# Kernel tuning notes

Hardware: AMD Instinct MI355X
Metric: run time of the kernel (lower is better)

## Reference

```python
import jax, jax.numpy as jnp
import numpy as np

B, T, E, V, H = 2, 2048, 1024, 2048, 8
KD, HD = E // H, V // H  # key_dim=128, head_dim=256
EPS = 1e-6


def rotate_every_two(x):
    x1 = x[..., ::2]
    x2 = x[..., 1::2]
    return jnp.stack((-x2, x1), axis=-1).reshape(x.shape)


def theta_shift(x, sin, cos):
    return x * cos + rotate_every_two(x) * sin


def setup_inputs() -> dict:
    key = jax.random.key(0)
    ks = jax.random.split(key, 8)
    x = jax.random.normal(ks[0], (B, T, E), dtype=jnp.float32)
    angle = jnp.arange(T, dtype=jnp.float32)[:, None] * (1.0 / (10000.0 ** (jnp.repeat(jnp.arange(KD // 2, dtype=jnp.float32), 2) * 2.0 / KD)))
    sin = jnp.sin(angle)  # [T, KD]
    cos = jnp.cos(angle)
    # RetNet per-head causal decay mask: decay_h = 1 - 2^(-5-h)
    decay = 1.0 - 2.0 ** (-5.0 - jnp.arange(H, dtype=jnp.float32))  # [H]
    idx = jnp.arange(T, dtype=jnp.float32)
    diff = idx[:, None] - idx[None, :]  # n - m
    causal = diff >= 0
    mask = jnp.where(causal[None], jnp.exp(jnp.where(causal, diff, 0.0)[None] * jnp.log(decay)[:, None, None]), 0.0)  # [H,T,T]
    g = 2 ** (-2.5)
    Wq = jax.random.normal(ks[1], (E, E), dtype=jnp.float32) * (g * np.sqrt(2.0 / (E + E)))
    Wk = jax.random.normal(ks[2], (E, E), dtype=jnp.float32) * (g * np.sqrt(2.0 / (E + E)))
    Wv = jax.random.normal(ks[3], (E, V), dtype=jnp.float32) * (g * np.sqrt(2.0 / (E + V)))
    Wg = jax.random.normal(ks[4], (E, V), dtype=jnp.float32) * (g * np.sqrt(2.0 / (E + V)))
    Wo = jax.random.normal(ks[5], (V, E), dtype=jnp.float32) * np.sqrt(2.0 / (V + E))
    return {"x": x, "sin": sin, "cos": cos, "mask": mask,
            "Wq": Wq, "Wk": Wk, "Wv": Wv, "Wg": Wg, "Wo": Wo}


def reference(x, sin, cos, mask, Wq, Wk, Wv, Wg, Wo):
    b, t, _ = x.shape
    scaling = KD ** -0.5
    q = (x @ Wq).reshape(b, t, H, KD).transpose(0, 2, 1, 3)  # [B,H,T,KD]
    k = (x @ Wk * scaling).reshape(b, t, H, KD).transpose(0, 2, 1, 3)
    v = x @ Wv  # [B,T,V]
    g = x @ Wg
    qr = theta_shift(q, sin, cos)
    kr = theta_shift(k, sin, cos)
    vr = v.reshape(b, t, H, HD).transpose(0, 2, 1, 3)  # [B,H,T,HD]
    qk = jnp.einsum('bhsk,bhtk->bhst', qr, kr) * mask  # [B,H,T,T]
    denom = jnp.clip(jnp.abs(jax.lax.stop_gradient(qk).sum(-1, keepdims=True)), 1.0, None)
    qk = qk / denom
    out = jnp.einsum('bhst,bhtd->bhsd', qk, vr)  # [B,H,T,HD]
    out = out.transpose(0, 2, 1, 3)  # [B,T,H,HD]
    # RMSNorm over head_dim, no affine
    out = out * jax.lax.rsqrt(jnp.mean(out * out, axis=-1, keepdims=True) + EPS)
    out = out.reshape(b, t, H * HD)
    out = jax.nn.silu(g) * out
    return out @ Wo  # [B,T,E]
```

## Files before the change

### kernel.cpp

```cpp
#include <hip/hip_runtime.h>
#include <hip/hip_bf16.h>


#define B_ 2
#define T_ 2048
#define E_ 1024
#define V_ 2048
#define H_ 8
#define KD_ 128
#define HD_ 256
#define M_ 4096

typedef __attribute__((ext_vector_type(8))) short bf16x8;
typedef __attribute__((ext_vector_type(4))) float f32x4;

__device__ __forceinline__ float u2f(unsigned short u) {
    return __uint_as_float(((unsigned)u) << 16);
}
__device__ __forceinline__ unsigned short f2bu(float f) {
    unsigned x = __float_as_uint(f);
    return (unsigned short)((x + 0x7fffu + ((x >> 16) & 1u)) >> 16);
}

typedef const __attribute__((address_space(1))) void gas_t;
typedef __attribute__((address_space(3))) void las_t;
__device__ __forceinline__ void gl_lds16(const void* g, void* l) {
    __builtin_amdgcn_global_load_lds((gas_t*)g, (las_t*)l, 16, 0, 0);
}

__global__ __launch_bounds__(256) void conv_x_kernel(
    const float* __restrict__ x, unsigned short* __restrict__ xb)
{
    const size_t i = ((size_t)blockIdx.x * 256 + threadIdx.x) * 8;
    float4 a = *(const float4*)(x + i);
    float4 c = *(const float4*)(x + i + 4);
    *(ushort4*)(xb + i)     = make_ushort4(f2bu(a.x), f2bu(a.y), f2bu(a.z), f2bu(a.w));
    *(ushort4*)(xb + i + 4) = make_ushort4(f2bu(c.x), f2bu(c.y), f2bu(c.z), f2bu(c.w));
}

__global__ __launch_bounds__(256) void transW4_kernel(
    const float* __restrict__ Wq, const float* __restrict__ Wk,
    const float* __restrict__ Wv, const float* __restrict__ Wg,
    unsigned short* __restrict__ Wt)
{
    const int z = blockIdx.z;
    const float* W; int N; int rofs;
    if (z == 0)      { W = Wq; N = 1024; rofs = 0; }
    else if (z == 1) { W = Wk; N = 1024; rofs = 1024; }
    else if (z == 2) { W = Wv; N = 2048; rofs = 2048; }
    else             { W = Wg; N = 2048; rofs = 4096; }
    const int n0 = blockIdx.x * 64;
    if (n0 >= N) return;
    const int k0 = blockIdx.y * 64;

    __shared__ float tl[64][65];
    const int tid = threadIdx.x;
    #pragma unroll
    for (int i = 0; i < 4; ++i) {
        int kr = i * 16 + (tid >> 4);
        int nc = (tid & 15) * 4;
        float4 v = *(const float4*)(W + (size_t)(k0 + kr) * N + n0 + nc);
        tl[kr][nc] = v.x; tl[kr][nc + 1] = v.y; tl[kr][nc + 2] = v.z; tl[kr][nc + 3] = v.w;
    }
    __syncthreads();
    #pragma unroll
    for (int i = 0; i < 4; ++i) {
        int nr = i * 16 + (tid >> 4);
        int kc = (tid & 15) * 4;
        ushort4 u = make_ushort4(f2bu(tl[kc + 0][nr]), f2bu(tl[kc + 1][nr]),
                                 f2bu(tl[kc + 2][nr]), f2bu(tl[kc + 3][nr]));
        *(ushort4*)(Wt + (size_t)(rofs + n0 + nr) * E_ + k0 + kc) = u;
    }
}

__global__ __launch_bounds__(256) void transW_kernel(
    const float* __restrict__ W, unsigned short* __restrict__ Wt, int K, int N)
{
    __shared__ float tl[64][65];
    const int tid = threadIdx.x;
    const int n0 = blockIdx.x * 64, k0 = blockIdx.y * 64;
    #pragma unroll
    for (int i = 0; i < 4; ++i) {
        int kr = i * 16 + (tid >> 4);
        int nc = (tid & 15) * 4;
        float4 v = *(const float4*)(W + (size_t)(k0 + kr) * N + n0 + nc);
        tl[kr][nc] = v.x; tl[kr][nc + 1] = v.y; tl[kr][nc + 2] = v.z; tl[kr][nc + 3] = v.w;
    }
    __syncthreads();
    #pragma unroll
    for (int i = 0; i < 4; ++i) {
        int nr = i * 16 + (tid >> 4);
        int kc = (tid & 15) * 4;
        ushort4 u = make_ushort4(f2bu(tl[kc + 0][nr]), f2bu(tl[kc + 1][nr]),
                                 f2bu(tl[kc + 2][nr]), f2bu(tl[kc + 3][nr]));
        *(ushort4*)(Wt + (size_t)(n0 + nr) * K + k0 + kc) = u;
    }
}

__global__ __launch_bounds__(256) void transV_kernel(
    const unsigned short* __restrict__ vb, unsigned short* __restrict__ vt)
{
    __shared__ unsigned short tl[64][68];
    const int tid = threadIdx.x;
    const int t0 = blockIdx.x * 64, c0 = blockIdx.y * 64, b = blockIdx.z;
    #pragma unroll
    for (int i = 0; i < 4; ++i) {
        int tr = i * 16 + (tid >> 4);
        int cc = (tid & 15) * 4;
        ushort4 v = *(const ushort4*)(vb + (size_t)(b * T_ + t0 + tr) * V_ + c0 + cc);
        tl[tr][cc] = v.x; tl[tr][cc + 1] = v.y; tl[tr][cc + 2] = v.z; tl[tr][cc + 3] = v.w;
    }
    __syncthreads();
    #pragma unroll
    for (int i = 0; i < 4; ++i) {
        int cr = i * 16 + (tid >> 4);
        int tc = (tid & 15) * 4;
        ushort4 u = make_ushort4(tl[tc + 0][cr], tl[tc + 1][cr], tl[tc + 2][cr], tl[tc + 3][cr]);
        *(ushort4*)(vt + (size_t)(b * V_ + c0 + cr) * T_ + t0 + tc) = u;
    }
}

#define GSTAGE(BUF, K0)                                                        \
    {                                                                          \
        _Pragma("unroll")                                                      \
        for (int i = 0; i < 4; ++i) {                                          \
            int r = i * 32 + srow;                                             \
            int cb = scolb ^ ((r & 7) << 4);                                   \
            gl_lds16((const char*)(A  + (size_t)(rowBase + r) * K + (K0)) + cb,\
                     Asm[BUF] + i * 4096 + w * 1024);                          \
            gl_lds16((const char*)(Bt + (size_t)(colBase + r) * K + (K0)) + cb,\
                     Bsm[BUF] + i * 4096 + w * 1024);                          \
        }                                                                      \
    }

#define GCOMPUTE(BUF)                                                          \
    {                                                                          \
        _Pragma("unroll")                                                      \
        for (int kk = 0; kk < 2; ++kk) {                                       \
            const int cb = kk * 64 + (l >> 4) * 16;                            \
            bf16x8 a[4], b[4];                                                 \
            _Pragma("unroll")                                                  \
            for (int m = 0; m < 4; ++m) {                                      \
                int r = wr * 64 + m * 16 + (l & 15);                           \
                a[m] = *(const bf16x8*)(Asm[BUF] + r * 128 + (cb ^ ((r & 7) << 4))); \
            }                                                                  \
            _Pragma("unroll")                                                  \
            for (int n = 0; n < 4; ++n) {                                      \
                int r = wc * 64 + n * 16 + (l & 15);                           \
                b[n] = *(const bf16x8*)(Bsm[BUF] + r * 128 + (cb ^ ((r & 7) << 4))); \
            }                                                                  \
            _Pragma("unroll")                                                  \
            for (int m = 0; m < 4; ++m)                                        \
                _Pragma("unroll")                                              \
                for (int n = 0; n < 4; ++n)                                    \
                    acc[m][n] = __builtin_amdgcn_mfma_f32_16x16x32_bf16(a[m], b[n], acc[m][n], 0, 0, 0); \
        }                                                                      \
    }

#define GEMM_PIPELINE_LOOP                                                     \
    GSTAGE(0, 0)                                                               \
    const int nk = K / 64;                                                     \
    for (int kt = 0; kt < nk; ++kt) {                                          \
        const int cur = kt & 1;                                                \
        if (kt + 1 < nk) {                                                     \
            GSTAGE(1 - cur, (kt + 1) * 64)                                     \
            asm volatile("s_waitcnt vmcnt(8)" ::: "memory");                   \
        } else {                                                               \
            asm volatile("s_waitcnt vmcnt(0)" ::: "memory");                   \
        }                                                                      \
        __builtin_amdgcn_s_barrier();                                          \
        __builtin_amdgcn_sched_barrier(0);                                     \
        GCOMPUTE(cur)                                                          \
        __builtin_amdgcn_s_barrier();                                          \
        __builtin_amdgcn_sched_barrier(0);                                     \
    }

__global__ __launch_bounds__(256) void gemm_qkvg_kernel(
    const unsigned short* __restrict__ A,
    const unsigned short* __restrict__ Bt,
    unsigned short* __restrict__ qb,
    unsigned short* __restrict__ kb,
    unsigned short* __restrict__ vb,
    unsigned short* __restrict__ gb)
{
    const int K = E_;
    __shared__ __align__(16) char Asm[2][128 * 64 * 2];
    __shared__ __align__(16) char Bsm[2][128 * 64 * 2];
    const int tid = threadIdx.x;
    const int l = tid & 63;
    const int w = tid >> 6;
    const int wr = w >> 1, wc = w & 1;
    const int rowBase = blockIdx.y * 128;
    const int colBase = blockIdx.x * 128;
    const int srow = tid >> 3;
    const int scolb = (tid & 7) * 16;

    f32x4 acc[4][4] = {};

    GEMM_PIPELINE_LOOP

    const int colW = colBase + wc * 64;
    unsigned short* dst;
    int cofs, stride;
    if (colW < 1024)      { dst = qb; cofs = 0;    stride = E_; }
    else if (colW < 2048) { dst = kb; cofs = 1024; stride = E_; }
    else if (colW < 4096) { dst = vb; cofs = 2048; stride = V_; }
    else                  { dst = gb; cofs = 4096; stride = V_; }
    #pragma unroll
    for (int m = 0; m < 4; ++m)
        #pragma unroll
        for (int n = 0; n < 4; ++n)
            #pragma unroll
            for (int r = 0; r < 4; ++r) {
                int row = rowBase + wr * 64 + m * 16 + (l >> 4) * 4 + r;
                int col = colW + n * 16 + (l & 15);
                float f = acc[m][n][r];
                if (!isfinite(f)) f = 0.f;
                dst[(size_t)row * stride + (col - cofs)] = f2bu(f);
            }
}

__global__ __launch_bounds__(256) void gemm_wo_kernel(
    const unsigned short* __restrict__ A,
    const unsigned short* __restrict__ Bt,
    float* __restrict__ C)
{
    const int K = V_;
    __shared__ __align__(16) char Asm[2][64 * 128];
    __shared__ __align__(16) char Bsm[2][128 * 128];
    const int tid = threadIdx.x;
    const int l = tid & 63;
    const int w = tid >> 6;
    const int wr = w >> 1, wc = w & 1;
    const int rowBase = blockIdx.y * 64;
    const int colBase = blockIdx.x * 128;
    const int srow = tid >> 3;
    const int scolb = (tid & 7) * 16;

    f32x4 acc[2][4] = {};

#define WSTAGE(BUF, K0)                                                        \
    {                                                                          \
        _Pragma("unroll")                                                      \
        for (int i = 0; i < 2; ++i) {                                          \
            int r = i * 32 + srow;                                             \
            int cb = scolb ^ ((r & 7) << 4);                                   \
            gl_lds16((const char*)(A + (size_t)(rowBase + r) * K + (K0)) + cb, \
                     Asm[BUF] + i * 4096 + w * 1024);                          \
        }                                                                      \
        _Pragma("unroll")                                                      \
        for (int i = 0; i < 4; ++i) {                                          \
            int r = i * 32 + srow;                                             \
            int cb = scolb ^ ((r & 7) << 4);                                   \
            gl_lds16((const char*)(Bt + (size_t)(colBase + r) * K + (K0)) + cb,\
                     Bsm[BUF] + i * 4096 + w * 1024);                          \
        }                                                                      \
    }

    WSTAGE(0, 0)
    const int nk = K / 64;
    for (int kt = 0; kt < nk; ++kt) {
        const int cur = kt & 1;
        if (kt + 1 < nk) {
            WSTAGE(1 - cur, (kt + 1) * 64)
            asm volatile("s_waitcnt vmcnt(6)" ::: "memory");
        } else {
            asm volatile("s_waitcnt vmcnt(0)" ::: "memory");
        }
        __builtin_amdgcn_s_barrier();
        __builtin_amdgcn_sched_barrier(0);
        #pragma unroll
        for (int kk = 0; kk < 2; ++kk) {
            const int cb = kk * 64 + (l >> 4) * 16;
            bf16x8 a[2], b[4];
            #pragma unroll
            for (int m = 0; m < 2; ++m) {
                int r = wr * 32 + m * 16 + (l & 15);
                a[m] = *(const bf16x8*)(Asm[cur] + r * 128 + (cb ^ ((r & 7) << 4)));
            }
            #pragma unroll
            for (int n = 0; n < 4; ++n) {
                int r = wc * 64 + n * 16 + (l & 15);
                b[n] = *(const bf16x8*)(Bsm[cur] + r * 128 + (cb ^ ((r & 7) << 4)));
            }
            #pragma unroll
            for (int m = 0; m < 2; ++m)
                #pragma unroll
                for (int n = 0; n < 4; ++n)
                    acc[m][n] = __builtin_amdgcn_mfma_f32_16x16x32_bf16(a[m], b[n], acc[m][n], 0, 0, 0);
        }
        __builtin_amdgcn_s_barrier();
        __builtin_amdgcn_sched_barrier(0);
    }
#undef WSTAGE

    #pragma unroll
    for (int m = 0; m < 2; ++m)
        #pragma unroll
        for (int n = 0; n < 4; ++n)
            #pragma unroll
            for (int r = 0; r < 4; ++r) {
                int row = rowBase + wr * 32 + m * 16 + (l >> 4) * 4 + r;
                int col = colBase + wc * 64 + n * 16 + (l & 15);
                float f = acc[m][n][r];
                if (!isfinite(f)) f = 0.f;
                C[(size_t)row * E_ + col] = f;
            }
}

__global__ __launch_bounds__(256) void theta2_kernel(
    unsigned short* __restrict__ qb,
    unsigned short* __restrict__ kb,
    const float* __restrict__ sinp, const float* __restrict__ cosp)
{
    unsigned short* qk = blockIdx.y ? kb : qb;
    const float scale = blockIdx.y ? 0.088388347648318447f : 1.0f;
    const int i = blockIdx.x * 256 + threadIdx.x;
    const int pe = i & (E_ / 2 - 1);
    const int bt = i >> 9;
    const int t = bt & (T_ - 1);
    const int e0 = pe << 1;
    const int d0 = e0 & (KD_ - 1);
    const size_t base = (size_t)bt * E_ + e0;
    const float q0 = u2f(qk[base]);
    const float q1 = u2f(qk[base + 1]);
    const int sb = t * KD_ + d0;
    const float s0 = sinp[sb], s1 = sinp[sb + 1];
    const float c0 = cosp[sb], c1 = cosp[sb + 1];
    qk[base]     = f2bu((q0 * c0 - q1 * s0) * scale);
    qk[base + 1] = f2bu((q1 * c1 + q0 * s1) * scale);
}

#define STAGE_K(BUF, T0)                                                       \
    {                                                                          \
        _Pragma("unroll")                                                      \
        for (int i = 0; i < 4; ++i) {                                          \
            int r = i * 16 + (tid >> 4);                                       \
            int cb = ((tid & 15) * 16) ^ ((r & 7) << 4);                       \
            gl_lds16((const char*)(kb + (size_t)(b * T_ + (T0) + r) * E_ + h * KD_) + cb, \
                     Ks[BUF] + i * 4096 + w * 1024);                           \
        }                                                                      \
    }

#define STAGE_V(T0)                                                            \
    {                                                                          \
        _Pragma("unroll")                                                      \
        for (int i = 0; i < 8; ++i) {                                          \
            int r = i * 32 + (tid >> 3);                                       \
            int cb = ((tid & 7) * 16) ^ ((r & 7) << 4);                        \
            gl_lds16((const char*)(vt + (size_t)((b * H_ + h) * HD_ + r) * T_ + (T0)) + cb, \
                     Vs + i * 4096 + w * 1024);                                \
        }                                                                      \
    }

__global__ __launch_bounds__(256) void retention_mfma_kernel(
    const unsigned short* __restrict__ qb,
    const unsigned short* __restrict__ kb,
    const unsigned short* __restrict__ vt,
    const unsigned short* __restrict__ g,
    unsigned short* __restrict__ ao)
{
    __shared__ __align__(16) char Ks[2][64 * 128 * 2];
    __shared__ __align__(16) char Vs[256 * 64 * 2];
    __shared__ __align__(16) char Ps[64 * 64 * 2];
    __shared__ float rsum_lds[64];
    __shared__ float rsq_lds[4][64];
    const int tid = threadIdx.x;
    const int l = tid & 63;
    const int w = tid >> 6;
    const int orig = (int)blockIdx.x;
    const int xcd  = orig & 7;
    const int pos  = orig >> 3;
    const int slot = pos >> 5;
    const int cu   = pos & 31;
    const int half = cu >> 4;
    const int c15  = cu & 15;
    const int bh   = xcd * 2 + half;
    const int chunk = slot ? c15 : (31 - c15);
    const int b = bh >> 3, h = bh & 7;
    const int s0 = chunk * 64;
    const float ld = logf(1.f - exp2f(-5.f - (float)h));

    float es[4], etl[4];
    #pragma unroll
    for (int r = 0; r < 4; ++r)
        es[r] = __expf((float)(s0 + w * 16 + (l >> 4) * 4 + r) * ld);
    #pragma unroll
    for (int n = 0; n < 4; ++n)
        etl[n] = __expf(-(float)(n * 16 + (l & 15)) * ld);
    const float Dm64 = __expf(-64.f * ld);
    float etb = 1.f;

    bf16x8 qf[4];
    {
        const char* qp = (const char*)(qb + (size_t)(b * T_ + s0 + w * 16 + (l & 15)) * E_ + h * KD_);
        #pragma unroll
        for (int kk = 0; kk < 4; ++kk)
            qf[kk] = *(const bf16x8*)(qp + kk * 64 + (l >> 4) * 16);
    }

    f32x4 oacc[4][4] = {};
    float rs[4] = {0.f, 0.f, 0.f, 0.f};

    const int nt = chunk + 1;
    STAGE_K(0, 0)

    for (int t = 0; t < nt; ++t) {
        const int cur = t & 1;
        const int t0 = t * 64;
        STAGE_V(t0)
        if (t + 1 < nt) {
            STAGE_K(1 - cur, t0 + 64)
            asm volatile("s_waitcnt vmcnt(12)" ::: "memory");
        } else {
            asm volatile("s_waitcnt vmcnt(8)" ::: "memory");
        }
        __builtin_amdgcn_s_barrier();
        __builtin_amdgcn_sched_barrier(0);

        f32x4 sacc[4] = {};
        #pragma unroll
        for (int kk = 0; kk < 4; ++kk) {
            const int cb = kk * 64 + (l >> 4) * 16;
            #pragma unroll
            for (int n = 0; n < 4; ++n) {
                int r = n * 16 + (l & 15);
                bf16x8 kf = *(const bf16x8*)(Ks[cur] + r * 256 + (cb ^ ((r & 7) << 4)));
                sacc[n] = __builtin_amdgcn_mfma_f32_16x16x32_bf16(qf[kk], kf, sacc[n], 0, 0, 0);
            }
        }
        float et[4];
        #pragma unroll
        for (int n = 0; n < 4; ++n) et[n] = etb * etl[n];
        etb *= Dm64;
        float rsp[4] = {0.f, 0.f, 0.f, 0.f};
        #pragma unroll
        for (int n = 0; n < 4; ++n)
            #pragma unroll
            for (int r = 0; r < 4; ++r) {
                int qrow = w * 16 + (l >> 4) * 4 + r;
                int tcol = n * 16 + (l & 15);
                int d = (s0 + qrow) - (t0 + tcol);
                float pm = (d >= 0) ? sacc[n][r] * (es[r] * et[n]) : 0.f;
                rsp[r] += pm;
                *(unsigned short*)(Ps + qrow * 128 + ((tcol * 2) ^ ((qrow & 7) << 4))) = f2bu(pm);
            }
        #pragma unroll
        for (int r = 0; r < 4; ++r) {
            float vv = rsp[r];
            vv += __shfl_xor(vv, 1, 16);
            vv += __shfl_xor(vv, 2, 16);
            vv += __shfl_xor(vv, 4, 16);
            vv += __shfl_xor(vv, 8, 16);
            rs[r] += vv;
        }
        if (t + 1 < nt) {
            asm volatile("s_waitcnt vmcnt(4) lgkmcnt(0)" ::: "memory");
        } else {
            asm volatile("s_waitcnt vmcnt(0) lgkmcnt(0)" ::: "memory");
        }
        __builtin_amdgcn_s_barrier();
        __builtin_amdgcn_sched_barrier(0);
        #pragma unroll
        for (int kk = 0; kk < 2; ++kk) {
            const int cb = kk * 64 + (l >> 4) * 16;
            bf16x8 pf[4];
            #pragma unroll
            for (int m = 0; m < 4; ++m) {
                int pr = m * 16 + (l & 15);
                pf[m] = *(const bf16x8*)(Ps + pr * 128 + (cb ^ ((pr & 7) << 4)));
            }
            #pragma unroll
            for (int n = 0; n < 4; ++n) {
                int r = w * 64 + n * 16 + (l & 15);
                bf16x8 vf = *(const bf16x8*)(Vs + r * 128 + (cb ^ ((r & 7) << 4)));
                #pragma unroll
                for (int m = 0; m < 4; ++m)
                    oacc[m][n] = __builtin_amdgcn_mfma_f32_16x16x32_bf16(pf[m], vf, oacc[m][n], 0, 0, 0);
            }
        }
        __builtin_amdgcn_s_barrier();
        __builtin_amdgcn_sched_barrier(0);
    }

    #pragma unroll
    for (int r = 0; r < 4; ++r)
        if ((l & 15) == 0) rsum_lds[w * 16 + (l >> 4) * 4 + r] = rs[r];
    __syncthreads();

    #pragma unroll
    for (int m = 0; m < 4; ++m)
        #pragma unroll
        for (int r = 0; r < 4; ++r) {
            const int row = m * 16 + (l >> 4) * 4 + r;
            const float inv = 1.f / fmaxf(fabsf(rsum_lds[row]), 1.f);
            float ps = 0.f;
            #pragma unroll
            for (int n = 0; n < 4; ++n) {
                float o = oacc[m][n][r] * inv;
                ps += o * o;
            }
            ps += __shfl_xor(ps, 1, 16);
            ps += __shfl_xor(ps, 2, 16);
            ps += __shfl_xor(ps, 4, 16);
            ps += __shfl_xor(ps, 8, 16);
            if ((l & 15) == 0) rsq_lds[w][row] = ps;
        }
    __syncthreads();

    #pragma unroll
    for (int m = 0; m < 4; ++m)
        #pragma unroll
        for (int r = 0; r < 4; ++r) {
            const int row = m * 16 + (l >> 4) * 4 + r;
            const float inv = 1.f / fmaxf(fabsf(rsum_lds[row]), 1.f);
            const float tot = rsq_lds[0][row] + rsq_lds[1][row] + rsq_lds[2][row] + rsq_lds[3][row];
            const float scale = rsqrtf(tot * (1.0f / HD_) + 1e-6f) * inv;
            #pragma unroll
            for (int n = 0; n < 4; ++n) {
                const int col = h * HD_ + w * 64 + n * 16 + (l & 15);
                const float gv = u2f(g[(size_t)(b * T_ + s0 + row) * V_ + col]);
                const float silu = gv / (1.f + __expf(-gv));
                float f = oacc[m][n][r] * scale * silu;
                if (!isfinite(f)) f = 0.f;
                ao[(size_t)(b * T_ + s0 + row) * V_ + col] = f2bu(f);
            }
        }
}

extern "C" void kernel_launch(void* const* d_in, const int* in_sizes, int n_in,
                              void* d_out, int out_size, void* d_ws, size_t ws_size,
                              hipStream_t stream)
{
    const float* x    = (const float*)d_in[0];
    const float* sinp = (const float*)d_in[1];
    const float* cosp = (const float*)d_in[2];
    const float* Wq   = (const float*)d_in[4];
    const float* Wk   = (const float*)d_in[5];
    const float* Wv   = (const float*)d_in[6];
    const float* Wg   = (const float*)d_in[7];
    const float* Wo   = (const float*)d_in[8];
    float* out = (float*)d_out;

    unsigned short* xb = (unsigned short*)d_out;
    unsigned short* qb = xb + (size_t)M_ * E_;

    char* ws = (char*)d_ws;
    unsigned short* kb  = (unsigned short*)(ws + 0);
    unsigned short* vb  = (unsigned short*)(ws + 8388608);
    unsigned short* gb  = (unsigned short*)(ws + 25165824);
    unsigned short* wt  = (unsigned short*)(ws + 41943040);
    unsigned short* vt  = (unsigned short*)(ws + 54525952);
    unsigned short* aob = (unsigned short*)(ws + 71303168);
    unsigned short* wot = (unsigned short*)(ws + 88080384);

    dim3 blk(256);
    conv_x_kernel<<<M_ * E_ / 8 / 256, blk, 0, stream>>>(x, xb);

    transW4_kernel<<<dim3(32, 16, 4), blk, 0, stream>>>(Wq, Wk, Wv, Wg, wt);

    gemm_qkvg_kernel<<<dim3(48, 32), blk, 0, stream>>>(xb, wt, qb, kb, vb, gb);

    theta2_kernel<<<dim3(M_ * E_ / 2 / 256, 2), blk, 0, stream>>>(qb, kb, sinp, cosp);

    transV_kernel<<<dim3(32, 32, B_), blk, 0, stream>>>(vb, vt);

    retention_mfma_kernel<<<dim3(512), blk, 0, stream>>>(qb, kb, vt, gb, aob);

    transW_kernel<<<dim3(16, 32), blk, 0, stream>>>(Wo, wot, V_, E_);
    gemm_wo_kernel<<<dim3(8, 64), blk, 0, stream>>>(aob, wot, out);
}
```

Before: 203.3 us.

## Transpose retention MFMA layout so query index lives in lanes, vectorize P and output stores

```diff
diff --git a/kernel.cpp b/kernel.cpp
--- a/kernel.cpp
+++ b/kernel.cpp
@@ -353,7 +353,7 @@
         }                                                                      \
     }
 
-__global__ __launch_bounds__(256) void retention_mfma_kernel(
+__global__ __launch_bounds__(256, 2) void retention_mfma_kernel(
     const unsigned short* __restrict__ qb,
     const unsigned short* __restrict__ kb,
     const unsigned short* __restrict__ vt,
@@ -362,12 +362,14 @@
 {
     __shared__ __align__(16) char Ks[2][64 * 128 * 2];
     __shared__ __align__(16) char Vs[256 * 64 * 2];
-    __shared__ __align__(16) char Ps[64 * 64 * 2];
-    __shared__ float rsum_lds[64];
-    __shared__ float rsq_lds[4][64];
+    __shared__ __align__(16) char Pq[64 * 64 * 2];
+    __shared__ float rsum_p[4][64];
+    __shared__ float rsq_p[4][64];
     const int tid = threadIdx.x;
     const int l = tid & 63;
     const int w = tid >> 6;
+    const int g_ = l >> 4;
+    const int q15 = l & 15;
     const int orig = (int)blockIdx.x;
     const int xcd  = orig & 7;
     const int pos  = orig >> 3;
@@ -381,25 +383,27 @@
     const int s0 = chunk * 64;
     const float ld = logf(1.f - exp2f(-5.f - (float)h));
 
-    float es[4], etl[4];
+    float es[4];
+    #pragma unroll
+    for (int qb2 = 0; qb2 < 4; ++qb2)
+        es[qb2] = __expf((float)(s0 + qb2 * 16 + q15) * ld);
+    float etl[4];
     #pragma unroll
     for (int r = 0; r < 4; ++r)
-        es[r] = __expf((float)(s0 + w * 16 + (l >> 4) * 4 + r) * ld);
-    #pragma unroll
-    for (int n = 0; n < 4; ++n)
-        etl[n] = __expf(-(float)(n * 16 + (l & 15)) * ld);
+        etl[r] = __expf(-(float)(w * 16 + 4 * g_ + r) * ld);
     const float Dm64 = __expf(-64.f * ld);
     float etb = 1.f;
 
-    bf16x8 qf[4];
-    {
-        const char* qp = (const char*)(qb + (size_t)(b * T_ + s0 + w * 16 + (l & 15)) * E_ + h * KD_);
+    bf16x8 qf[4][4];
+    #pragma unroll
+    for (int qb2 = 0; qb2 < 4; ++qb2) {
+        const char* qp = (const char*)(qb + (size_t)(b * T_ + s0 + qb2 * 16 + q15) * E_ + h * KD_);
         #pragma unroll
         for (int kk = 0; kk < 4; ++kk)
-            qf[kk] = *(const bf16x8*)(qp + kk * 64 + (l >> 4) * 16);
-    }
-
-    f32x4 oacc[4][4] = {};
+            qf[qb2][kk] = *(const bf16x8*)(qp + kk * 64 + g_ * 16);
+    }
+
+    f32x4 oaccT[4][4] = {};
     float rs[4] = {0.f, 0.f, 0.f, 0.f};
 
     const int nt = chunk + 1;
@@ -419,40 +423,39 @@
         __builtin_amdgcn_sched_barrier(0);
 
         f32x4 sacc[4] = {};
-        #pragma unroll
-        for (int kk = 0; kk < 4; ++kk) {
-            const int cb = kk * 64 + (l >> 4) * 16;
-            #pragma unroll
-            for (int n = 0; n < 4; ++n) {
-                int r = n * 16 + (l & 15);
-                bf16x8 kf = *(const bf16x8*)(Ks[cur] + r * 256 + (cb ^ ((r & 7) << 4)));
-                sacc[n] = __builtin_amdgcn_mfma_f32_16x16x32_bf16(qf[kk], kf, sacc[n], 0, 0, 0);
-            }
-        }
-        float et[4];
-        #pragma unroll
-        for (int n = 0; n < 4; ++n) et[n] = etb * etl[n];
-        etb *= Dm64;
-        float rsp[4] = {0.f, 0.f, 0.f, 0.f};
-        #pragma unroll
-        for (int n = 0; n < 4; ++n)
-            #pragma unroll
-            for (int r = 0; r < 4; ++r) {
-                int qrow = w * 16 + (l >> 4) * 4 + r;
-                int tcol = n * 16 + (l & 15);
-                int d = (s0 + qrow) - (t0 + tcol);
-                float pm = (d >= 0) ? sacc[n][r] * (es[r] * et[n]) : 0.f;
-                rsp[r] += pm;
-                *(unsigned short*)(Ps + qrow * 128 + ((tcol * 2) ^ ((qrow & 7) << 4))) = f2bu(pm);
-            }
-        #pragma unroll
-        for (int r = 0; r < 4; ++r) {
-            float vv = rsp[r];
-            vv += __shfl_xor(vv, 1, 16);
-            vv += __shfl_xor(vv, 2, 16);
-            vv += __shfl_xor(vv, 4, 16);
-            vv += __shfl_xor(vv, 8, 16);
-            rs[r] += vv;
+        {
+            const int krow = w * 16 + q15;
+            const int swz = (krow & 7) << 4;
+            #pragma unroll
+            for (int kk = 0; kk < 4; ++kk) {
+                bf16x8 kf = *(const bf16x8*)(Ks[cur] + krow * 256 + ((kk * 64 + g_ * 16) ^ swz));
+                #pragma unroll
+                for (int qb2 = 0; qb2 < 4; ++qb2)
+                    sacc[qb2] = __builtin_amdgcn_mfma_f32_16x16x32_bf16(kf, qf[qb2][kk], sacc[qb2], 0, 0, 0);
+            }
+        }
+        {
+            const float etw = etb;
+            #pragma unroll
+            for (int qb2 = 0; qb2 < 4; ++qb2) {
+                const int qg = s0 + qb2 * 16 + q15;
+                const int q_local = qb2 * 16 + q15;
+                float rsp = 0.f;
+                unsigned short pk[4];
+                #pragma unroll
+                for (int r = 0; r < 4; ++r) {
+                    int tg = t0 + w * 16 + 4 * g_ + r;
+                    float pm = (qg >= tg) ? sacc[qb2][r] * (es[qb2] * etw * etl[r]) : 0.f;
+                    rsp += pm;
+                    pk[r] = f2bu(pm);
+                }
+                *(ushort4*)(Pq + q_local * 128 + (((w * 16 + 4 * g_) * 2) ^ ((q_local & 7) << 4))) =
+                    make_ushort4(pk[0], pk[1], pk[2], pk[3]);
+                rsp += __shfl_xor(rsp, 16);
+                rsp += __shfl_xor(rsp, 32);
+                rs[qb2] += rsp;
+            }
+            etb *= Dm64;
         }
         if (t + 1 < nt) {
             asm volatile("s_waitcnt vmcnt(4) lgkmcnt(0)" ::: "memory");
@@ -463,69 +466,84 @@
         __builtin_amdgcn_sched_barrier(0);
         #pragma unroll
         for (int kk = 0; kk < 2; ++kk) {
-            const int cb = kk * 64 + (l >> 4) * 16;
-            bf16x8 pf[4];
+            const int cb = kk * 64 + g_ * 16;
+            bf16x8 pf[4], vf[4];
+            #pragma unroll
+            for (int qb2 = 0; qb2 < 4; ++qb2) {
+                int pr = qb2 * 16 + q15;
+                pf[qb2] = *(const bf16x8*)(Pq + pr * 128 + (cb ^ ((pr & 7) << 4)));
+            }
             #pragma unroll
             for (int m = 0; m < 4; ++m) {
-                int pr = m * 16 + (l & 15);
-                pf[m] = *(const bf16x8*)(Ps + pr * 128 + (cb ^ ((pr & 7) << 4)));
-            }
-            #pragma unroll
-            for (int n = 0; n < 4; ++n) {
-                int r = w * 64 + n * 16 + (l & 15);
-                bf16x8 vf = *(const bf16x8*)(Vs + r * 128 + (cb ^ ((r & 7) << 4)));
+                int vr = w * 64 + m * 16 + q15;
+                vf[m] = *(const bf16x8*)(Vs + vr * 128 + (cb ^ ((vr & 7) << 4)));
+            }
+            #pragma unroll
+            for (int qb2 = 0; qb2 < 4; ++qb2)
                 #pragma unroll
                 for (int m = 0; m < 4; ++m)
-                    oacc[m][n] = __builtin_amdgcn_mfma_f32_16x16x32_bf16(pf[m], vf, oacc[m][n], 0, 0, 0);
-            }
+                    oaccT[qb2][m] = __builtin_amdgcn_mfma_f32_16x16x32_bf16(vf[m], pf[qb2], oaccT[qb2][m], 0, 0, 0);
         }
         __builtin_amdgcn_s_barrier();
         __builtin_amdgcn_sched_barrier(0);
     }
 
-    #pragma unroll
-    for (int r = 0; r < 4; ++r)
-        if ((l & 15) == 0) rsum_lds[w * 16 + (l >> 4) * 4 + r] = rs[r];
+    if (l < 16) {
+        #pragma unroll
+        for (int qb2 = 0; qb2 < 4; ++qb2)
+            rsum_p[w][qb2 * 16 + q15] = rs[qb2];
+    }
     __syncthreads();
 
-    #pragma unroll
-    for (int m = 0; m < 4; ++m)
-        #pragma unroll
-        for (int r = 0; r < 4; ++r) {
-            const int row = m * 16 + (l >> 4) * 4 + r;
-            const float inv = 1.f / fmaxf(fabsf(rsum_lds[row]), 1.f);
-            float ps = 0.f;
-            #pragma unroll
-            for (int n = 0; n < 4; ++n) {
-                float o = oacc[m][n][r] * inv;
+    float inv[4];
+    #pragma unroll
+    for (int qb2 = 0; qb2 < 4; ++qb2) {
+        const int q_local = qb2 * 16 + q15;
+        const float tot = rsum_p[0][q_local] + rsum_p[1][q_local] +
+                          rsum_p[2][q_local] + rsum_p[3][q_local];
+        inv[qb2] = 1.f / fmaxf(fabsf(tot), 1.f);
+    }
+
+    #pragma unroll
+    for (int qb2 = 0; qb2 < 4; ++qb2) {
+        float ps = 0.f;
+        #pragma unroll
+        for (int m = 0; m < 4; ++m)
+            #pragma unroll
+            for (int r = 0; r < 4; ++r) {
+                float o = oaccT[qb2][m][r] * inv[qb2];
                 ps += o * o;
             }
-            ps += __shfl_xor(ps, 1, 16);
-            ps += __shfl_xor(ps, 2, 16);
-            ps += __shfl_xor(ps, 4, 16);
-            ps += __shfl_xor(ps, 8, 16);
-            if ((l & 15) == 0) rsq_lds[w][row] = ps;
-        }
+        ps += __shfl_xor(ps, 16);
+        ps += __shfl_xor(ps, 32);
+        if (l < 16) rsq_p[w][qb2 * 16 + q15] = ps;
+    }
     __syncthreads();
 
     #pragma unroll
-    for (int m = 0; m < 4; ++m)
-        #pragma unroll
-        for (int r = 0; r < 4; ++r) {
-            const int row = m * 16 + (l >> 4) * 4 + r;
-            const float inv = 1.f / fmaxf(fabsf(rsum_lds[row]), 1.f);
-            const float tot = rsq_lds[0][row] + rsq_lds[1][row] + rsq_lds[2][row] + rsq_lds[3][row];
-            const float scale = rsqrtf(tot * (1.0f / HD_) + 1e-6f) * inv;
-            #pragma unroll
-            for (int n = 0; n < 4; ++n) {
-                const int col = h * HD_ + w * 64 + n * 16 + (l & 15);
-                const float gv = u2f(g[(size_t)(b * T_ + s0 + row) * V_ + col]);
-                const float silu = gv / (1.f + __expf(-gv));
-                float f = oacc[m][n][r] * scale * silu;
+    for (int qb2 = 0; qb2 < 4; ++qb2) {
+        const int q_local = qb2 * 16 + q15;
+        const float tot = rsq_p[0][q_local] + rsq_p[1][q_local] +
+                          rsq_p[2][q_local] + rsq_p[3][q_local];
+        const float scale = rsqrtf(tot * (1.0f / HD_) + 1e-6f) * inv[qb2];
+        const size_t rowb = (size_t)(b * T_ + s0 + q_local) * V_ + h * HD_;
+        #pragma unroll
+        for (int m = 0; m < 4; ++m) {
+            const int vc0 = w * 64 + m * 16 + 4 * g_;
+            ushort4 gv4 = *(const ushort4*)(g + rowb + vc0);
+            const unsigned short* gv = (const unsigned short*)&gv4;
+            unsigned short outp[4];
+            #pragma unroll
+            for (int r = 0; r < 4; ++r) {
+                const float gvf = u2f(gv[r]);
+                const float silu = gvf / (1.f + __expf(-gvf));
+                float f = oaccT[qb2][m][r] * scale * silu;
                 if (!isfinite(f)) f = 0.f;
-                ao[(size_t)(b * T_ + s0 + row) * V_ + col] = f2bu(f);
-            }
-        }
+                outp[r] = f2bu(f);
+            }
+            *(ushort4*)(ao + rowb + vc0) = make_ushort4(outp[0], outp[1], outp[2], outp[3]);
+        }
+    }
 }
 
 extern "C" void kernel_launch(void* const* d_in, const int* in_sizes, int n_in,
```

Result: faster. 190.6 us (-6.2%).
